# Kernel optimization log

Hardware: AMD Instinct MI355X
Metric: run time of the kernel (lower is better)

The kernel has to match this reference:

```python
import jax, jax.numpy as jnp
import numpy as np

K = 16            # number of nearest neighbors (module init arg)
NUM_CLASSES = 100 # label vocabulary size (matches labels fill_max)


def setup_inputs() -> dict:
    key = jax.random.key(0)
    k1, k2 = jax.random.split(key)
    distances = jax.random.normal(k1, (8192, 16384), dtype=jnp.float32)
    labels = jax.random.randint(k2, (16384,), 0, NUM_CLASSES, dtype=jnp.int64)
    return {"distances": distances, "labels": labels}


def reference(distances, labels):
    # top-k smallest distances == top-k of negated distances
    _, idx = jax.lax.top_k(-distances, K)          # idx: [B, K]
    winning_labels = labels[idx]                    # [B, K]
    # majority vote; torch.mode picks the smallest value among ties,
    # argmax over class-count picks the first (lowest) class among ties.
    counts = jax.nn.one_hot(winning_labels, NUM_CLASSES, dtype=jnp.int32).sum(axis=1)  # [B, C]
    return jnp.argmax(counts, axis=1)               # [B] predicted class per query
```

## Files before the change

kernel.cpp:

```cpp
#include <hip/hip_runtime.h>
#include <stdint.h>

#define COLS 16384
#define POOLCAP 256
typedef unsigned long long u64;
typedef float vf4 __attribute__((ext_vector_type(4)));

__device__ __forceinline__ uint32_t f2key(float x) {
  uint32_t u = __float_as_uint(x);
  u ^= (uint32_t)((int32_t)u >> 31) | 0x80000000u;
  return u;
}

__global__ __launch_bounds__(256, 4) void KNNC_20272245637217_kernel(
    const float* __restrict__ dist,
    const int* __restrict__ labels,
    int* __restrict__ out) {
  const int wave = threadIdx.x >> 6;
  const int lane = threadIdx.x & 63;
  const int row  = blockIdx.x * 4 + wave;

  __shared__ u64 poolK[4][POOLCAP];
  __shared__ int cnt[4];
  if (threadIdx.x < 4) cnt[threadIdx.x] = 0;
  __syncthreads();

  const vf4* __restrict__ rp = (const vf4*)(dist + (size_t)row * COLS);

  vf4 A8[8], B8[8];
#define LOAD8(b, buf) { _Pragma("unroll") \
  for (int u = 0; u < 8; ++u) (buf)[u] = __builtin_nontemporal_load(rp + (b)*512 + u*64 + lane); }

  LOAD8(0, A8)
  LOAD8(1, B8)

  float m = __builtin_inff();
  #pragma unroll
  for (int u = 0; u < 8; ++u)
    m = fminf(m, fminf(fminf(A8[u].x, A8[u].y), fminf(A8[u].z, A8[u].w)));
  #pragma unroll
  for (int u = 0; u < 8; ++u)
    m = fminf(m, fminf(fminf(B8[u].x, B8[u].y), fminf(B8[u].z, B8[u].w)));

  float v = m;
  #pragma unroll
  for (int k = 2; k <= 64; k <<= 1) {
    #pragma unroll
    for (int j = k >> 1; j >= 1; j >>= 1) {
      float o = __shfl_xor(v, j);
      bool keepMin = (((lane & j) == 0) == ((lane & k) == 0));
      v = keepMin ? fminf(v, o) : fmaxf(v, o);
    }
  }
  const float T = __shfl(v, 15);

#define PUSH(x, c) { if ((x) <= T) { \
    int _s = atomicAdd(&cnt[wave], 1); \
    if (_s < POOLCAP) poolK[wave][_s] = (((u64)f2key(x)) << 32) | (u64)(uint32_t)(c); } }
#define PROC8(buf, b) { _Pragma("unroll") \
  for (int u = 0; u < 8; ++u) { \
    vf4 w = (buf)[u]; \
    float mn = fminf(fminf(w.x, w.y), fminf(w.z, w.w)); \
    if (mn <= T) { \
      int col = ((b)*8 + u) * 256 + lane * 4; \
      PUSH(w.x, col) PUSH(w.y, col+1) PUSH(w.z, col+2) PUSH(w.w, col+3) \
    } } }

  PROC8(A8, 0)
  LOAD8(2, A8)
  PROC8(B8, 1)
  LOAD8(3, B8)
  PROC8(A8, 2)
  LOAD8(4, A8)
  PROC8(B8, 3)
  LOAD8(5, B8)
  PROC8(A8, 4)
  LOAD8(6, A8)
  PROC8(B8, 5)
  LOAD8(7, B8)
  PROC8(A8, 6)
  PROC8(B8, 7)

  __syncthreads();

  int C = cnt[wave];
  if (C > POOLCAP) C = POOLCAP;

  u64 key[4];
  #pragma unroll
  for (int t = 0; t < 4; ++t) {
    int p = lane + 64 * t;
    key[t] = (p < C) ? poolK[wave][p] : ~0ULL;
  }

  u64 myWin = ~0ULL;
  for (int r = 0; r < 16; ++r) {
    u64 k = key[0];
    k = (key[1] < k) ? key[1] : k;
    k = (key[2] < k) ? key[2] : k;
    k = (key[3] < k) ? key[3] : k;
    #pragma unroll
    for (int off = 32; off >= 1; off >>= 1) {
      u64 o = __shfl_xor(k, off);
      k = (o < k) ? o : k;
    }
    if (lane == r) myWin = k;
    #pragma unroll
    for (int t = 0; t < 4; ++t)
      if (key[t] == k) key[t] = ~0ULL;
  }

  int myLabel = 0;
  if (lane < 16) myLabel = labels[(uint32_t)myWin];

  int c = 0;
  #pragma unroll
  for (int s = 0; s < 16; ++s) {
    int ls = __shfl(myLabel, s);
    c += (ls == myLabel) ? 1 : 0;
  }
  int vkey = (lane < 16) ? ((c << 7) | (127 - myLabel)) : 0;
  #pragma unroll
  for (int off = 32; off >= 1; off >>= 1) {
    int o = __shfl_xor(vkey, off);
    vkey = (o > vkey) ? o : vkey;
  }
  if (lane == 0) out[row] = 127 - (vkey & 127);
}

extern "C" void kernel_launch(void* const* d_in, const int* in_sizes, int n_in,
                              void* d_out, int out_size, void* d_ws, size_t ws_size,
                              hipStream_t stream) {
  const float* dist   = (const float*)d_in[0];
  const int*   labels = (const int*)d_in[1];
  int*         out    = (int*)d_out;
  const int rows = out_size;
  KNNC_20272245637217_kernel<<<rows / 4, 256, 0, stream>>>(dist, labels, out);
}
```

Measured before the change: 665.4 us.

## Stream row tail through an LDS ring via direct global-to-LDS loads

```diff
diff --git a/kernel.cpp b/kernel.cpp
--- a/kernel.cpp
+++ b/kernel.cpp
@@ -2,7 +2,9 @@
 #include <stdint.h>
 
 #define COLS 16384
-#define POOLCAP 256
+#define POOLCAP 248
+#define RING 8
+#define NCHUNK 48
 typedef unsigned long long u64;
 typedef float vf4 __attribute__((ext_vector_type(4)));
 
@@ -20,12 +22,14 @@
   const int lane = threadIdx.x & 63;
   const int row  = blockIdx.x * 4 + wave;
 
+  __shared__ vf4 ringv[4][RING][64];
   __shared__ u64 poolK[4][POOLCAP];
   __shared__ int cnt[4];
   if (threadIdx.x < 4) cnt[threadIdx.x] = 0;
   __syncthreads();
 
-  const vf4* __restrict__ rp = (const vf4*)(dist + (size_t)row * COLS);
+  const float* __restrict__ rowp = dist + (size_t)row * COLS;
+  const vf4* __restrict__ rp = (const vf4*)rowp;
 
   vf4 A8[8], B8[8];
 #define LOAD8(b, buf) { _Pragma("unroll") \
@@ -33,6 +37,15 @@
 
   LOAD8(0, A8)
   LOAD8(1, B8)
+
+#define ISSUE(c) __builtin_amdgcn_global_load_lds( \
+    (const __attribute__((address_space(1))) void*)(rowp + 4096 + (c) * 256 + lane * 4), \
+    (__attribute__((address_space(3))) void*)(&ringv[wave][(c) & (RING - 1)][0]), \
+    16, 0, 0);
+
+  #pragma unroll
+  for (int c = 0; c < RING; ++c) { ISSUE(c) }
+  __builtin_amdgcn_sched_barrier(0);
 
   float m = __builtin_inff();
   #pragma unroll
@@ -67,19 +80,25 @@
     } } }
 
   PROC8(A8, 0)
-  LOAD8(2, A8)
   PROC8(B8, 1)
-  LOAD8(3, B8)
-  PROC8(A8, 2)
-  LOAD8(4, A8)
-  PROC8(B8, 3)
-  LOAD8(5, B8)
-  PROC8(A8, 4)
-  LOAD8(6, A8)
-  PROC8(B8, 5)
-  LOAD8(7, B8)
-  PROC8(A8, 6)
-  PROC8(B8, 7)
+
+#define RPROC(i, W) { \
+    asm volatile("s_waitcnt vmcnt(" #W ")" ::: "memory"); \
+    vf4 w = ringv[wave][(i) & (RING - 1)][lane]; \
+    float mn = fminf(fminf(w.x, w.y), fminf(w.z, w.w)); \
+    if (mn <= T) { \
+      int col = 4096 + (i) * 256 + lane * 4; \
+      PUSH(w.x, col) PUSH(w.y, col+1) PUSH(w.z, col+2) PUSH(w.w, col+3) \
+    } }
+
+  #pragma unroll 8
+  for (int i = 0; i < NCHUNK - RING; ++i) {
+    RPROC(i, 7)
+    asm volatile("s_waitcnt lgkmcnt(0)" ::: "memory");
+    ISSUE(i + RING)
+  }
+  RPROC(40, 7) RPROC(41, 6) RPROC(42, 5) RPROC(43, 4)
+  RPROC(44, 3) RPROC(45, 2) RPROC(46, 1) RPROC(47, 0)
 
   __syncthreads();
 
```

Result: slower. 695.9 us (+4.6%).

## Process one row per block with a block-wide threshold instead of one row per wave

Applied to the files above, without the earlier changes.

```diff
diff --git a/kernel.cpp b/kernel.cpp
--- a/kernel.cpp
+++ b/kernel.cpp
@@ -2,7 +2,8 @@
 #include <stdint.h>
 
 #define COLS 16384
-#define POOLCAP 256
+#define VPT 16
+#define POOLCAP 320
 typedef unsigned long long u64;
 typedef float vf4 __attribute__((ext_vector_type(4)));
 
@@ -16,31 +17,28 @@
     const float* __restrict__ dist,
     const int* __restrict__ labels,
     int* __restrict__ out) {
-  const int wave = threadIdx.x >> 6;
-  const int lane = threadIdx.x & 63;
-  const int row  = blockIdx.x * 4 + wave;
+  const int tid  = threadIdx.x;
+  const int wave = tid >> 6;
+  const int lane = tid & 63;
+  const int row  = blockIdx.x;
 
-  __shared__ u64 poolK[4][POOLCAP];
-  __shared__ int cnt[4];
-  if (threadIdx.x < 4) cnt[threadIdx.x] = 0;
+  __shared__ u64   poolK[POOLCAP];
+  __shared__ float tmin[64];
+  __shared__ float Tsh;
+  __shared__ int   cnt;
+  if (tid == 0) cnt = 0;
   __syncthreads();
 
   const vf4* __restrict__ rp = (const vf4*)(dist + (size_t)row * COLS);
 
-  vf4 A8[8], B8[8];
-#define LOAD8(b, buf) { _Pragma("unroll") \
-  for (int u = 0; u < 8; ++u) (buf)[u] = __builtin_nontemporal_load(rp + (b)*512 + u*64 + lane); }
-
-  LOAD8(0, A8)
-  LOAD8(1, B8)
+  vf4 V[VPT];
+  #pragma unroll
+  for (int i = 0; i < VPT; ++i) V[i] = rp[tid + 256 * i];
 
   float m = __builtin_inff();
   #pragma unroll
-  for (int u = 0; u < 8; ++u)
-    m = fminf(m, fminf(fminf(A8[u].x, A8[u].y), fminf(A8[u].z, A8[u].w)));
-  #pragma unroll
-  for (int u = 0; u < 8; ++u)
-    m = fminf(m, fminf(fminf(B8[u].x, B8[u].y), fminf(B8[u].z, B8[u].w)));
+  for (int i = 0; i < VPT; ++i)
+    m = fminf(m, fminf(fminf(V[i].x, V[i].y), fminf(V[i].z, V[i].w)));
 
   float v = m;
   #pragma unroll
@@ -52,80 +50,84 @@
       v = keepMin ? fminf(v, o) : fmaxf(v, o);
     }
   }
-  const float T = __shfl(v, 15);
+  if (lane < 16) tmin[wave * 16 + lane] = v;
+  __syncthreads();
+
+  if (wave == 0) {
+    float w = tmin[lane];
+    #pragma unroll
+    for (int k = 2; k <= 64; k <<= 1) {
+      #pragma unroll
+      for (int j = k >> 1; j >= 1; j >>= 1) {
+        float o = __shfl_xor(w, j);
+        bool keepMin = (((lane & j) == 0) == ((lane & k) == 0));
+        w = keepMin ? fminf(w, o) : fmaxf(w, o);
+      }
+    }
+    if (lane == 15) Tsh = w;
+  }
+  __syncthreads();
+  const float T = Tsh;
 
 #define PUSH(x, c) { if ((x) <= T) { \
-    int _s = atomicAdd(&cnt[wave], 1); \
-    if (_s < POOLCAP) poolK[wave][_s] = (((u64)f2key(x)) << 32) | (u64)(uint32_t)(c); } }
-#define PROC8(buf, b) { _Pragma("unroll") \
-  for (int u = 0; u < 8; ++u) { \
-    vf4 w = (buf)[u]; \
-    float mn = fminf(fminf(w.x, w.y), fminf(w.z, w.w)); \
-    if (mn <= T) { \
-      int col = ((b)*8 + u) * 256 + lane * 4; \
-      PUSH(w.x, col) PUSH(w.y, col+1) PUSH(w.z, col+2) PUSH(w.w, col+3) \
-    } } }
+    int _s = atomicAdd(&cnt, 1); \
+    if (_s < POOLCAP) poolK[_s] = (((u64)f2key(x)) << 32) | (u64)(uint32_t)(c); } }
 
-  PROC8(A8, 0)
-  LOAD8(2, A8)
-  PROC8(B8, 1)
-  LOAD8(3, B8)
-  PROC8(A8, 2)
-  LOAD8(4, A8)
-  PROC8(B8, 3)
-  LOAD8(5, B8)
-  PROC8(A8, 4)
-  LOAD8(6, A8)
-  PROC8(B8, 5)
-  LOAD8(7, B8)
-  PROC8(A8, 6)
-  PROC8(B8, 7)
-
+  #pragma unroll
+  for (int i = 0; i < VPT; ++i) {
+    vf4 w = V[i];
+    float mn = fminf(fminf(w.x, w.y), fminf(w.z, w.w));
+    if (mn <= T) {
+      int col = (tid + 256 * i) * 4;
+      PUSH(w.x, col) PUSH(w.y, col + 1) PUSH(w.z, col + 2) PUSH(w.w, col + 3)
+    }
+  }
   __syncthreads();
 
-  int C = cnt[wave];
-  if (C > POOLCAP) C = POOLCAP;
+  if (wave == 0) {
+    int C = cnt;
+    if (C > POOLCAP) C = POOLCAP;
 
-  u64 key[4];
-  #pragma unroll
-  for (int t = 0; t < 4; ++t) {
-    int p = lane + 64 * t;
-    key[t] = (p < C) ? poolK[wave][p] : ~0ULL;
-  }
+    u64 key[5];
+    #pragma unroll
+    for (int t = 0; t < 5; ++t) {
+      int p = lane + 64 * t;
+      key[t] = (p < C) ? poolK[p] : ~0ULL;
+    }
 
-  u64 myWin = ~0ULL;
-  for (int r = 0; r < 16; ++r) {
-    u64 k = key[0];
-    k = (key[1] < k) ? key[1] : k;
-    k = (key[2] < k) ? key[2] : k;
-    k = (key[3] < k) ? key[3] : k;
+    u64 myWin = ~0ULL;
+    for (int r = 0; r < 16; ++r) {
+      u64 k = key[0];
+      #pragma unroll
+      for (int t = 1; t < 5; ++t) k = (key[t] < k) ? key[t] : k;
+      #pragma unroll
+      for (int off = 32; off >= 1; off >>= 1) {
+        u64 o = __shfl_xor(k, off);
+        k = (o < k) ? o : k;
+      }
+      if (lane == r) myWin = k;
+      #pragma unroll
+      for (int t = 0; t < 5; ++t)
+        if (key[t] == k) key[t] = ~0ULL;
+    }
+
+    int myLabel = 0;
+    if (lane < 16) myLabel = labels[(uint32_t)myWin];
+
+    int c = 0;
+    #pragma unroll
+    for (int s = 0; s < 16; ++s) {
+      int ls = __shfl(myLabel, s);
+      c += (ls == myLabel) ? 1 : 0;
+    }
+    int vkey = (lane < 16) ? ((c << 7) | (127 - myLabel)) : 0;
     #pragma unroll
     for (int off = 32; off >= 1; off >>= 1) {
-      u64 o = __shfl_xor(k, off);
-      k = (o < k) ? o : k;
+      int o = __shfl_xor(vkey, off);
+      vkey = (o > vkey) ? o : vkey;
     }
-    if (lane == r) myWin = k;
-    #pragma unroll
-    for (int t = 0; t < 4; ++t)
-      if (key[t] == k) key[t] = ~0ULL;
+    if (lane == 0) out[row] = 127 - (vkey & 127);
   }
-
-  int myLabel = 0;
-  if (lane < 16) myLabel = labels[(uint32_t)myWin];
-
-  int c = 0;
-  #pragma unroll
-  for (int s = 0; s < 16; ++s) {
-    int ls = __shfl(myLabel, s);
-    c += (ls == myLabel) ? 1 : 0;
-  }
-  int vkey = (lane < 16) ? ((c << 7) | (127 - myLabel)) : 0;
-  #pragma unroll
-  for (int off = 32; off >= 1; off >>= 1) {
-    int o = __shfl_xor(vkey, off);
-    vkey = (o > vkey) ? o : vkey;
-  }
-  if (lane == 0) out[row] = 127 - (vkey & 127);
 }
 
 extern "C" void kernel_launch(void* const* d_in, const int* in_sizes, int n_in,
@@ -135,5 +137,5 @@
   const int*   labels = (const int*)d_in[1];
   int*         out    = (int*)d_out;
   const int rows = out_size;
-  KNNC_20272245637217_kernel<<<rows / 4, 256, 0, stream>>>(dist, labels, out);
+  KNNC_20272245637217_kernel<<<rows, 256, 0, stream>>>(dist, labels, out);
 }
```

Measured after the change: 681.7 us. 1.02x slower.
